# Kernel optimization log

Measured on AMD Instinct MI355X. Metric: run time of the kernel, lower is better.

## Reference

```python
import jax, jax.numpy as jnp
import numpy as np

N = 10000      # nodes
E = 160000     # edges (before self-loops)
F_IN = 128     # num_features
H1, D1 = 4, 256   # conv1: 4 heads x 256, concat -> 1024
D2 = 256          # conv2: 1 head x 256
NEG_SLOPE = 0.2


def setup_inputs() -> dict:
    key = jax.random.key(0)
    ks = jax.random.split(key, 12)
    def p(k, shape, fan):
        return jax.random.normal(k, shape, jnp.float32) / np.float32(np.sqrt(fan))
    return {
        "x": jax.random.normal(ks[0], (N, F_IN), jnp.float32),
        "edge_index": jax.random.randint(ks[1], (2, E), 0, N, jnp.int32),
        "W1": p(ks[2], (F_IN, H1 * D1), F_IN),
        "att_src1": p(ks[3], (H1, D1), D1),
        "att_dst1": p(ks[4], (H1, D1), D1),
        "b1": jnp.zeros((H1 * D1,), jnp.float32),
        "lin1_W": p(ks[5], (F_IN, H1 * D1), F_IN),
        "lin1_b": jnp.zeros((H1 * D1,), jnp.float32),
        "W2": p(ks[6], (H1 * D1, D2), H1 * D1),
        "att_src2": p(ks[7], (1, D2), D2),
        "att_dst2": p(ks[8], (1, D2), D2),
        "b2": jnp.zeros((D2,), jnp.float32),
        "lin2_W": p(ks[9], (H1 * D1, D2), H1 * D1),
        "lin2_b": jnp.zeros((D2,), jnp.float32),
    }


def gat_layer(x, src, dst, W, a_src, a_dst, b, heads, d):
    """PyG-style GATConv: transform, edgewise LeakyReLU attention,
    segment-softmax over destination neighborhoods, scatter-add, concat heads."""
    n = x.shape[0]
    h = (x @ W).reshape(n, heads, d)                       # [N, H, D]
    s_src = jnp.einsum('nhd,hd->nh', h, a_src)             # per-node scores
    s_dst = jnp.einsum('nhd,hd->nh', h, a_dst)
    e = jax.nn.leaky_relu(s_src[src] + s_dst[dst], NEG_SLOPE)   # [E, H]
    m = jax.ops.segment_max(e, dst, num_segments=n)        # stable softmax per dst
    p = jnp.exp(e - m[dst])
    z = jax.ops.segment_sum(p, dst, num_segments=n)
    alpha = p / (z[dst] + 1e-16)                           # [E, H]
    msg = h[src] * alpha[:, :, None]                       # [E, H, D]
    out = jax.ops.segment_sum(msg, dst, num_segments=n)    # [N, H, D]
    return out.reshape(n, heads * d) + b, alpha


def reference(x, edge_index, W1, att_src1, att_dst1, b1, lin1_W, lin1_b,
              W2, att_src2, att_dst2, b2, lin2_W, lin2_b):
    n = x.shape[0]
    loop = jnp.arange(n, dtype=edge_index.dtype)           # add self-loops (PyG default)
    src = jnp.concatenate([edge_index[0], loop])
    dst = jnp.concatenate([edge_index[1], loop])
    h1, alpha1 = gat_layer(x, src, dst, W1, att_src1, att_dst1, b1, H1, D1)
    h1 = jax.nn.elu(h1 + x @ lin1_W + lin1_b)              # conv1 + lin1 residual, ELU
    h2, _ = gat_layer(h1, src, dst, W2, att_src2, att_dst2, b2, 1, D2)
    out = h2 + h1 @ lin2_W + lin2_b                        # conv2 + lin2 residual
    return out, alpha1
```

## Files before the change

kernel.cpp:

```cpp
#include <hip/hip_runtime.h>
#include <hip/hip_bf16.h>
#include <math.h>

#define NN   10000
#define EE   160000
#define ETOT 170000
#define FIN  128
#define C1   1024
#define NH1  4
#define D1   256
#define D2   256

typedef __attribute__((ext_vector_type(8))) short bf16x8;
typedef __attribute__((ext_vector_type(4))) float f32x4;

__device__ __forceinline__ float b2f(unsigned short u)
{
    union { unsigned int i; float f; } c; c.i = (unsigned int)u << 16; return c.f;
}
__device__ __forceinline__ unsigned short f2b(float x)
{
    return __builtin_bit_cast(unsigned short, __float2bfloat16(x));
}
__device__ __forceinline__ void split1(float x, unsigned short &h, unsigned short &l)
{
    __hip_bfloat16 hb = __float2bfloat16(x);
    float r = x - __bfloat162float(hb);
    h = __builtin_bit_cast(unsigned short, hb);
    l = __builtin_bit_cast(unsigned short, __float2bfloat16(r));
}

__device__ __forceinline__ void split_A_body(const float* __restrict__ X,
                                             unsigned short* __restrict__ A2,
                                             int M, int K, int idx)
{
    int kq4 = K >> 2;
    if (idx >= M * kq4) return;
    int m = idx / kq4, kq = idx % kq4;
    float4 v = *(const float4*)&X[(size_t)m * K + kq * 4];
    ushort4 h, l;
    split1(v.x, h.x, l.x); split1(v.y, h.y, l.y);
    split1(v.z, h.z, l.z); split1(v.w, h.w, l.w);
    unsigned short* row = A2 + (size_t)m * (2 * K);
    *(ushort4*)&row[kq * 4]     = h;
    *(ushort4*)&row[K + kq * 4] = l;
}

__device__ __forceinline__ void split_Bt_body(const float* __restrict__ B0,
                                              const float* __restrict__ B1,
                                              int K, int N0, int Ntot,
                                              unsigned short* __restrict__ Bt, int idx)
{
    int total = Ntot * (K >> 2);
    if (idx >= total) return;
    int n = idx % Ntot;
    int kq = idx / Ntot;
    int k = kq * 4;
    const float* B; int nc, nb;
    if (n < N0) { B = B0; nc = n; nb = N0; }
    else        { B = B1; nc = n - N0; nb = Ntot - N0; }
    float v0 = B[(size_t)(k + 0) * nb + nc];
    float v1 = B[(size_t)(k + 1) * nb + nc];
    float v2 = B[(size_t)(k + 2) * nb + nc];
    float v3 = B[(size_t)(k + 3) * nb + nc];
    ushort4 h, l;
    split1(v0, h.x, l.x); split1(v1, h.y, l.y);
    split1(v2, h.z, l.z); split1(v3, h.w, l.w);
    unsigned short* row = Bt + (size_t)n * (3 * K);
    *(ushort4*)&row[k]         = h;
    *(ushort4*)&row[K + k]     = h;
    *(ushort4*)&row[2 * K + k] = l;
}

__device__ __forceinline__ void split_Bt1_body(const float* __restrict__ W1,
                                               const float* __restrict__ lin1W,
                                               unsigned short* __restrict__ Bt, int idx)
{
    if (idx >= 1024 * 64) return;
    int n = idx & 1023;
    int k = (idx >> 10) * 4;
    float v[4];
    #pragma unroll
    for (int i = 0; i < 4; ++i) {
        int kk = k + i;
        v[i] = (kk < 128) ? W1[(size_t)kk * C1 + n] : lin1W[(size_t)(kk - 128) * C1 + n];
    }
    ushort4 h, l;
    split1(v[0], h.x, l.x); split1(v[1], h.y, l.y);
    split1(v[2], h.z, l.z); split1(v[3], h.w, l.w);
    unsigned short* row = Bt + (size_t)n * 768;
    *(ushort4*)&row[k]       = h;
    *(ushort4*)&row[256 + k] = h;
    *(ushort4*)&row[512 + k] = l;
}

__global__ __launch_bounds__(256)
void prep(const float* __restrict__ x, unsigned short* __restrict__ A1stk,
          const float* __restrict__ W1, const float* __restrict__ lin1_W,
          unsigned short* __restrict__ Bt1,
          const float* __restrict__ W2, const float* __restrict__ lin2_W,
          unsigned short* __restrict__ Bt2,
          const int* __restrict__ dstp, int* __restrict__ cnt,
          const float* __restrict__ as1, const float* __restrict__ ad1,
          float* __restrict__ w1s, float* __restrict__ w1d,
          const float* __restrict__ as2, const float* __restrict__ ad2,
          float* __restrict__ v2s, float* __restrict__ v2d)
{
    const int b = blockIdx.x, t = threadIdx.x;
    const int w = t >> 6, lane = t & 63;
    if (b < 1250) {
        split_A_body(x, A1stk, NN, FIN, b * 256 + t);
    } else if (b < 1506) {
        split_Bt1_body(W1, lin1_W, Bt1, (b - 1250) * 256 + t);
    } else if (b < 2018) {
        split_Bt_body(W2, lin2_W, C1, D2, 512, Bt2, (b - 1506) * 256 + t);
    } else if (b < 2683) {
        int e = (b - 2018) * 256 + t;
        if (e < ETOT) {
            int d = (e < EE) ? dstp[e] : (e - EE);
            atomicAdd(&cnt[d], 1);
        }
    } else if (b < 2939) {
        int gw = (b - 2683) * 4 + w;
        int k = gw >> 3, rem = gw & 7, h = rem >> 1, issd = rem & 1;
        const float* a = issd ? ad1 : as1;
        float4 wv = *(const float4*)&W1[(size_t)k * C1 + h * 256 + lane * 4];
        float4 av = *(const float4*)&a[h * 256 + lane * 4];
        float s = wv.x * av.x + wv.y * av.y + wv.z * av.z + wv.w * av.w;
        #pragma unroll
        for (int off = 32; off; off >>= 1) s += __shfl_xor(s, off);
        if (lane == 0) (issd ? w1d : w1s)[k * 4 + h] = s;
    } else {
        int gw = (b - 2939) * 4 + w;
        int k = gw >> 1, issd = gw & 1;
        const float* a = issd ? ad2 : as2;
        float4 wv = *(const float4*)&W2[(size_t)k * D2 + lane * 4];
        float4 av = *(const float4*)&a[lane * 4];
        float s = wv.x * av.x + wv.y * av.y + wv.z * av.z + wv.w * av.w;
        #pragma unroll
        for (int off = 32; off; off >>= 1) s += __shfl_xor(s, off);
        if (lane == 0) (issd ? v2d : v2s)[k] = s;
    }
}

__device__ __forceinline__ void glds16(const void* g, void* l)
{
    __builtin_amdgcn_global_load_lds((const __attribute__((address_space(1))) void*)g,
                                     (__attribute__((address_space(3))) void*)l, 16, 0, 0);
}

__global__ __launch_bounds__(256)
void gemm_l1(const unsigned short* __restrict__ Apx,
             const unsigned short* __restrict__ Ax,
             const unsigned short* __restrict__ Bt,
             unsigned short* __restrict__ h1split,
             int M, const float* __restrict__ bias0, const float* __restrict__ bias1)
{
    constexpr int BM = 128, BN = 128, BK = 32;
    constexpr int FJ = 4, FI = 4;
    constexpr int SLOTS = 4, SMASK = 3, SWSH = 1;
    constexpr int RPC = 16, ACH = 8, CPW = 4;
    constexpr int ABUF = BM * BK, BBUF = BN * BK;
    __shared__ __align__(16) unsigned short sA[2 * ABUF];
    __shared__ __align__(16) unsigned short sB[2 * BBUF];
    const int tid = threadIdx.x, w = tid >> 6, lane = tid & 63;
    const int cpx = gridDim.x >> 3;
    const int t0 = (blockIdx.x & 7) * cpx + (blockIdx.x >> 3);
    const int m0 = (t0 >> 3) * BM;
    const int n0 = (t0 & 7) * BN;
    const int hsel = n0 >> 8;
    const int wm = w >> 1, wn = w & 1;
    f32x4 acc[FI][FJ] = {};

    const unsigned short *gx[CPW], *gpx[CPW], *gb[CPW];
    int lofs[CPW]; bool isa[CPW];
    {
        const int r = lane / SLOTS, sl = lane % SLOTS;
        const int ssl = sl ^ ((r >> SWSH) & SMASK);
        #pragma unroll
        for (int cc = 0; cc < CPW; ++cc) {
            int c = w * CPW + cc;
            if (c < ACH) {
                int gm = m0 + c * RPC + r; if (gm >= M) gm = M - 1;
                gx[cc]  = Ax  + (size_t)gm * 256 + ssl * 8;
                gpx[cc] = Apx + (size_t)gm * 1024 + hsel * 256 + ssl * 8;
                gb[cc]  = nullptr;
                lofs[cc] = c * 512;
                isa[cc] = true;
            } else {
                int gn = n0 + (c - ACH) * RPC + r;
                gx[cc] = gpx[cc] = nullptr;
                gb[cc] = Bt + (size_t)gn * 768 + ssl * 8;
                lofs[cc] = (c - ACH) * 512;
                isa[cc] = false;
            }
        }
    }

    const int rAl = wm * 64 + (lane & 15);
    const int rBl = wn * 64 + (lane & 15);
    const int sIdx = lane >> 4;
    const int nit = 768 / BK;
    int cur = 0;

    auto stage = [&](int kk, int buf) {
        int rr = kk >> 7;
        bool px = !(rr & 1);
        int off = px ? ((rr == 2) ? 128 : 0) : ((rr == 3) ? 128 : 0);
        int kin = kk & 127;
        #pragma unroll
        for (int cc = 0; cc < CPW; ++cc) {
            if (isa[cc]) glds16((px ? gpx[cc] : gx[cc]) + off + kin, sA + buf * ABUF + lofs[cc]);
            else         glds16(gb[cc] + kk,                         sB + buf * BBUF + lofs[cc]);
        }
    };

    stage(0, 0);
    __syncthreads();
    for (int it = 0; it < nit; ++it) {
        if (it + 1 < nit) stage((it + 1) * BK, cur ^ 1);
        const unsigned short* cA = sA + cur * ABUF;
        const unsigned short* cB = sB + cur * BBUF;
        bf16x8 av[FJ], bv[FI];
        #pragma unroll
        for (int f = 0; f < FI; ++f) {
            int row = rBl + f * 16;
            bv[f] = *(const bf16x8*)&cB[row * BK + ((sIdx ^ ((row >> SWSH) & SMASK)) << 3)];
        }
        #pragma unroll
        for (int f = 0; f < FJ; ++f) {
            int row = rAl + f * 16;
            av[f] = *(const bf16x8*)&cA[row * BK + ((sIdx ^ ((row >> SWSH) & SMASK)) << 3)];
        }
        #pragma unroll
        for (int fj = 0; fj < FJ; ++fj)
            #pragma unroll
            for (int fi = 0; fi < FI; ++fi)
                acc[fi][fj] = __builtin_amdgcn_mfma_f32_16x16x32_bf16(
                    bv[fi], av[fj], acc[fi][fj], 0, 0, 0);
        __syncthreads();
        cur ^= 1;
    }

    const int lrow = lane & 15;
    const int lcol = (lane >> 4) << 2;
    #pragma unroll
    for (int fj = 0; fj < FJ; ++fj) {
        int row = m0 + wm * 64 + fj * 16 + lrow;
        if (row >= M) continue;
        #pragma unroll
        for (int fi = 0; fi < FI; ++fi) {
            int col = n0 + wn * 64 + fi * 16 + lcol;
            f32x4 v = acc[fi][fj];
            const float4 g0 = *(const float4*)&bias0[col];
            const float4 g1 = *(const float4*)&bias1[col];
            v[0] += g0.x + g1.x; v[1] += g0.y + g1.y;
            v[2] += g0.z + g1.z; v[3] += g0.w + g1.w;
            #pragma unroll
            for (int i = 0; i < 4; ++i) v[i] = v[i] > 0.f ? v[i] : expm1f(v[i]);
            ushort4 hi, lo;
            split1(v[0], hi.x, lo.x); split1(v[1], hi.y, lo.y);
            split1(v[2], hi.z, lo.z); split1(v[3], hi.w, lo.w);
            unsigned short* orow = h1split + (size_t)row * 2048;
            *(ushort4*)&orow[col]        = hi;
            *(ushort4*)&orow[C1 + col]   = lo;
        }
    }
}

template<int BM, int BN, int WM, int WN, int BK>
__global__ __launch_bounds__(256)
void gemm_split(const unsigned short* __restrict__ A, int lda, int ka2,
                const unsigned short* __restrict__ Bt, int keff,
                unsigned short* __restrict__ outPb, float* __restrict__ outR,
                int M, int nsplit, int ldR, int ntn,
                const float* __restrict__ bias0, const float* __restrict__ bias1)
{
    constexpr int WTM  = BM / WM,  WTN = BN / WN;
    constexpr int FJ   = WTM / 16, FI  = WTN / 16;
    constexpr int KS   = BK / 32;
    constexpr int SLOTS = BK / 8;
    constexpr int SMASK = SLOTS - 1;
    constexpr int SWSH  = (BK == 32) ? 1 : 0;
    constexpr int RPC  = 512 / BK;
    constexpr int ACH  = BM / RPC;
    constexpr int NCH  = (BM + BN) / RPC;
    constexpr int CPW  = NCH / 4;
    constexpr int ABUF = BM * BK, BBUF = BN * BK;

    __shared__ __align__(16) unsigned short sA[2 * ABUF];
    __shared__ __align__(16) unsigned short sB[2 * BBUF];

    const int tid = threadIdx.x;
    const int w = tid >> 6, lane = tid & 63;

    const int cpx = gridDim.x >> 3;
    const int t0  = (blockIdx.x & 7) * cpx + (blockIdx.x >> 3);
    const int m0 = (t0 / ntn) * BM;
    const int n0 = (t0 % ntn) * BN;
    const int wm = w / WN, wn = w % WN;

    f32x4 acc[FI][FJ] = {};

    const unsigned short* gp[CPW];
    int lofs[CPW];
    bool isa[CPW];
    {
        const int r  = lane / SLOTS;
        const int sl = lane % SLOTS;
        const int ssl = sl ^ ((r >> SWSH) & SMASK);
        #pragma unroll
        for (int cc = 0; cc < CPW; ++cc) {
            int c = w * CPW + cc;
            if (c < ACH) {
                int gm = m0 + c * RPC + r; if (gm >= M) gm = M - 1;
                gp[cc]   = A + (size_t)gm * lda + ssl * 8;
                lofs[cc] = c * 512;
                isa[cc]  = true;
            } else {
                int gn = n0 + (c - ACH) * RPC + r;
                gp[cc]   = Bt + (size_t)gn * keff + ssl * 8;
                lofs[cc] = (c - ACH) * 512;
                isa[cc]  = false;
            }
        }
    }

    const int rAl = wm * WTM + (lane & 15);
    const int rBl = wn * WTN + (lane & 15);
    const int koff = (lane >> 4) * 8;
    const int nit = keff / BK;
    int cur = 0;

    #pragma unroll
    for (int cc = 0; cc < CPW; ++cc)
        glds16(gp[cc], (isa[cc] ? sA : sB) + lofs[cc]);
    __syncthreads();

    for (int it = 0; it < nit; ++it) {
        if (it + 1 < nit) {
            int kn = (it + 1) * BK;
            int kAn = (kn >= ka2) ? (kn - ka2) : kn;
            #pragma unroll
            for (int cc = 0; cc < CPW; ++cc) {
                unsigned short* dst = (isa[cc] ? sA + (cur ^ 1) * ABUF
                                               : sB + (cur ^ 1) * BBUF) + lofs[cc];
                glds16(gp[cc] + (isa[cc] ? kAn : kn), dst);
            }
        }
        const unsigned short* cA = sA + cur * ABUF;
        const unsigned short* cB = sB + cur * BBUF;
        #pragma unroll
        for (int ks = 0; ks < KS; ++ks) {
            const int sIdx = (ks * 32 + koff) >> 3;
            bf16x8 av[FJ], bv[FI];
            #pragma unroll
            for (int f = 0; f < FI; ++f) {
                int row = rBl + f * 16;
                bv[f] = *(const bf16x8*)&cB[row * BK + ((sIdx ^ ((row >> SWSH) & SMASK)) << 3)];
            }
            #pragma unroll
            for (int f = 0; f < FJ; ++f) {
                int row = rAl + f * 16;
                av[f] = *(const bf16x8*)&cA[row * BK + ((sIdx ^ ((row >> SWSH) & SMASK)) << 3)];
            }
            #pragma unroll
            for (int fj = 0; fj < FJ; ++fj)
                #pragma unroll
                for (int fi = 0; fi < FI; ++fi)
                    acc[fi][fj] = __builtin_amdgcn_mfma_f32_16x16x32_bf16(
                        bv[fi], av[fj], acc[fi][fj], 0, 0, 0);
        }
        __syncthreads();
        cur ^= 1;
    }

    const int lrow = lane & 15;
    const int lcol = (lane >> 4) << 2;
    #pragma unroll
    for (int fj = 0; fj < FJ; ++fj) {
        int row = m0 + wm * WTM + fj * 16 + lrow;
        if (row >= M) continue;
        #pragma unroll
        for (int fi = 0; fi < FI; ++fi) {
            int col = n0 + wn * WTN + fi * 16 + lcol;
            f32x4 v = acc[fi][fj];
            if (col < nsplit) {
                ushort4 o;
                o.x = f2b(v[0]); o.y = f2b(v[1]); o.z = f2b(v[2]); o.w = f2b(v[3]);
                *(ushort4*)&outPb[(size_t)row * nsplit + col] = o;
            } else {
                int c = col - nsplit;
                const float4 g0 = *(const float4*)&bias0[c];
                const float4 g1 = *(const float4*)&bias1[c];
                v[0] += g0.x + g1.x; v[1] += g0.y + g1.y;
                v[2] += g0.z + g1.z; v[3] += g0.w + g1.w;
                *(f32x4*)&outR[(size_t)row * ldR + c] = v;
            }
        }
    }
}

__global__ __launch_bounds__(256)
void s1_scores(const float* __restrict__ x, const float* __restrict__ w1s,
               const float* __restrict__ w1d, float* __restrict__ s_src,
               float* __restrict__ s_dst)
{
    const int n = blockIdx.x * 4 + (threadIdx.x >> 6);
    if (n >= NN) return;
    const int lane = threadIdx.x & 63;
    float2 xv = *(const float2*)&x[(size_t)n * FIN + lane * 2];
    float4 wa = *(const float4*)&w1s[(lane * 2) * 4];
    float4 wb = *(const float4*)&w1s[(lane * 2 + 1) * 4];
    float4 da = *(const float4*)&w1d[(lane * 2) * 4];
    float4 db = *(const float4*)&w1d[(lane * 2 + 1) * 4];
    float ss[4] = { xv.x * wa.x + xv.y * wb.x, xv.x * wa.y + xv.y * wb.y,
                    xv.x * wa.z + xv.y * wb.z, xv.x * wa.w + xv.y * wb.w };
    float sd[4] = { xv.x * da.x + xv.y * db.x, xv.x * da.y + xv.y * db.y,
                    xv.x * da.z + xv.y * db.z, xv.x * da.w + xv.y * db.w };
    #pragma unroll
    for (int off = 32; off; off >>= 1) {
        #pragma unroll
        for (int h = 0; h < 4; ++h) {
            ss[h] += __shfl_xor(ss[h], off);
            sd[h] += __shfl_xor(sd[h], off);
        }
    }
    if (lane == 0) {
        #pragma unroll
        for (int h = 0; h < 4; ++h) {
            s_src[n * NH1 + h] = ss[h];
            s_dst[n * NH1 + h] = sd[h];
        }
    }
}

__global__ __launch_bounds__(256)
void scores2(const unsigned short* __restrict__ h1split, const float* __restrict__ v2s,
             const float* __restrict__ v2d, float* __restrict__ s_src,
             float* __restrict__ s_dst)
{
    const int n = blockIdx.x * 4 + (threadIdx.x >> 6);
    if (n >= NN) return;
    const int lane = threadIdx.x & 63;
    const unsigned short* row = h1split + (size_t)n * 2048 + lane * 16;
    float ss = 0.f, sd = 0.f;
    #pragma unroll
    for (int q = 0; q < 16; ++q) {
        float hv = b2f(row[q]);
        ss += hv * v2s[lane * 16 + q];
        sd += hv * v2d[lane * 16 + q];
    }
    #pragma unroll
    for (int off = 32; off; off >>= 1) {
        ss += __shfl_xor(ss, off);
        sd += __shfl_xor(sd, off);
    }
    if (lane == 0) { s_src[n] = ss; s_dst[n] = sd; }
}

__global__ __launch_bounds__(1024)
void scan_kernel(const int* __restrict__ cnt, int* __restrict__ row_ptr)
{
    __shared__ int part[1024];
    const int t = threadIdx.x;
    int local[10];
    int s = 0;
    #pragma unroll
    for (int j = 0; j < 10; ++j) {
        int idx = t * 10 + j;
        local[j] = s;
        s += (idx < NN) ? cnt[idx] : 0;
    }
    part[t] = s;
    __syncthreads();
    for (int off = 1; off < 1024; off <<= 1) {
        int v = (t >= off) ? part[t - off] : 0;
        __syncthreads();
        part[t] += v;
        __syncthreads();
    }
    int prefix = (t > 0) ? part[t - 1] : 0;
    #pragma unroll
    for (int j = 0; j < 10; ++j) {
        int idx = t * 10 + j;
        if (idx < NN) row_ptr[idx] = prefix + local[j];
    }
    if (t == 0) row_ptr[NN] = ETOT;
}

__global__ void scatter_edges(const int* __restrict__ srcp, const int* __restrict__ dstp,
                              const int* __restrict__ row_ptr, int* __restrict__ fill,
                              int* __restrict__ csr_src, int* __restrict__ csr_eid,
                              int* __restrict__ csr_dst,
                              const float* __restrict__ s_src1,
                              const float* __restrict__ s_dst1,
                              float* __restrict__ sc1)
{
    int e = blockIdx.x * 256 + threadIdx.x;
    if (e >= ETOT) return;
    int s, d;
    if (e < EE) { s = srcp[e]; d = dstp[e]; } else { s = d = e - EE; }
    int pos = row_ptr[d] + atomicAdd(&fill[d], 1);
    csr_src[pos] = s;
    csr_eid[pos] = e;
    csr_dst[pos] = d;
    float4 ss = *(const float4*)&s_src1[s * 4];
    float4 dd = *(const float4*)&s_dst1[d * 4];
    float4 sc;
    sc.x = ss.x + dd.x; sc.y = ss.y + dd.y;
    sc.z = ss.z + dd.z; sc.w = ss.w + dd.w;
    sc.x = sc.x > 0.f ? sc.x : 0.2f * sc.x;
    sc.y = sc.y > 0.f ? sc.y : 0.2f * sc.y;
    sc.z = sc.z > 0.f ? sc.z : 0.2f * sc.z;
    sc.w = sc.w > 0.f ? sc.w : 0.2f * sc.w;
    *(float4*)&sc1[(size_t)pos * 4] = sc;
}

__global__ void sc2_kernel(const int* __restrict__ csr_src, const int* __restrict__ csr_dst,
                           const float* __restrict__ s_src2, const float* __restrict__ s_dst2,
                           float* __restrict__ sc2)
{
    int j = blockIdx.x * 256 + threadIdx.x;
    if (j >= ETOT) return;
    float sc = s_src2[csr_src[j]] + s_dst2[csr_dst[j]];
    sc2[j] = sc > 0.f ? sc : 0.2f * sc;
}

__global__ __launch_bounds__(256)
void mz1_alpha(const float* __restrict__ sc1, const int* __restrict__ row_ptr,
               const int* __restrict__ csr_eid, float* __restrict__ mz1,
               float* __restrict__ alpha_out)
{
    const int n = blockIdx.x * 4 + (threadIdx.x >> 6);
    if (n >= NN) return;
    const int lane = threadIdx.x & 63;
    const int start = row_ptr[n], end = row_ptr[n + 1];
    float4 m = make_float4(-1e30f, -1e30f, -1e30f, -1e30f);
    for (int i = start + lane; i < end; i += 64) {
        float4 s = *(const float4*)&sc1[(size_t)i * 4];
        m.x = fmaxf(m.x, s.x); m.y = fmaxf(m.y, s.y);
        m.z = fmaxf(m.z, s.z); m.w = fmaxf(m.w, s.w);
    }
    #pragma unroll
    for (int off = 32; off; off >>= 1) {
        m.x = fmaxf(m.x, __shfl_xor(m.x, off));
        m.y = fmaxf(m.y, __shfl_xor(m.y, off));
        m.z = fmaxf(m.z, __shfl_xor(m.z, off));
        m.w = fmaxf(m.w, __shfl_xor(m.w, off));
    }
    float4 z = make_float4(0.f, 0.f, 0.f, 0.f);
    for (int i = start + lane; i < end; i += 64) {
        float4 s = *(const float4*)&sc1[(size_t)i * 4];
        z.x += __expf(s.x - m.x); z.y += __expf(s.y - m.y);
        z.z += __expf(s.z - m.z); z.w += __expf(s.w - m.w);
    }
    #pragma unroll
    for (int off = 32; off; off >>= 1) {
        z.x += __shfl_xor(z.x, off); z.y += __shfl_xor(z.y, off);
        z.z += __shfl_xor(z.z, off); z.w += __shfl_xor(z.w, off);
    }
    float4 iz;
    iz.x = 1.f / (z.x + 1e-16f); iz.y = 1.f / (z.y + 1e-16f);
    iz.z = 1.f / (z.z + 1e-16f); iz.w = 1.f / (z.w + 1e-16f);
    if (lane == 0) {
        *(float4*)&mz1[(size_t)n * 8]     = m;
        *(float4*)&mz1[(size_t)n * 8 + 4] = iz;
    }
    for (int i = start + lane; i < end; i += 64) {
        float4 s = *(const float4*)&sc1[(size_t)i * 4];
        float4 a;
        a.x = __expf(s.x - m.x) * iz.x;
        a.y = __expf(s.y - m.y) * iz.y;
        a.z = __expf(s.z - m.z) * iz.z;
        a.w = __expf(s.w - m.w) * iz.w;
        *(float4*)&alpha_out[(size_t)csr_eid[i] * 4] = a;
    }
}

__global__ __launch_bounds__(256)
void mz2_kernel(const float* __restrict__ sc2, const int* __restrict__ row_ptr,
                float* __restrict__ mz2)
{
    const int n = blockIdx.x * 4 + (threadIdx.x >> 6);
    if (n >= NN) return;
    const int lane = threadIdx.x & 63;
    const int start = row_ptr[n], end = row_ptr[n + 1];
    float m = -1e30f;
    for (int i = start + lane; i < end; i += 64) m = fmaxf(m, sc2[i]);
    #pragma unroll
    for (int off = 32; off; off >>= 1) m = fmaxf(m, __shfl_xor(m, off));
    float z = 0.f;
    for (int i = start + lane; i < end; i += 64) z += __expf(sc2[i] - m);
    #pragma unroll
    for (int off = 32; off; off >>= 1) z += __shfl_xor(z, off);
    if (lane == 0) {
        mz2[(size_t)n * 2]     = m;
        mz2[(size_t)n * 2 + 1] = 1.f / (z + 1e-16f);
    }
}

__global__ __launch_bounds__(256)
void px_gather(const float* __restrict__ x, const float* __restrict__ sc1,
               const float* __restrict__ mz1, const int* __restrict__ row_ptr,
               const int* __restrict__ csr_src, unsigned short* __restrict__ Apx)
{
    __shared__ float red[4][16][33];
    const int n = blockIdx.x;
    const int t = threadIdx.x;
    const int w = t >> 6;
    const int lane = t & 63;
    const int start = row_ptr[n], end = row_ptr[n + 1];
    const float4 m  = *(const float4*)&mz1[(size_t)n * 8];
    const float4 iz = *(const float4*)&mz1[(size_t)n * 8 + 4];

    const int slot = w * 4 + (lane >> 4);
    const int g = lane & 15;
    float acc[4][8] = {};
    for (int i = start + slot; i < end; i += 16) {
        const int s = csr_src[i];
        float4 sv = *(const float4*)&sc1[(size_t)i * 4];
        const float a0 = __expf(sv.x - m.x) * iz.x;
        const float a1 = __expf(sv.y - m.y) * iz.y;
        const float a2 = __expf(sv.z - m.z) * iz.z;
        const float a3 = __expf(sv.w - m.w) * iz.w;
        const float* xr = &x[(size_t)s * FIN + g * 8];
        float4 v0 = *(const float4*)&xr[0];
        float4 v1 = *(const float4*)&xr[4];
        float vv[8] = { v0.x, v0.y, v0.z, v0.w, v1.x, v1.y, v1.z, v1.w };
        #pragma unroll
        for (int d = 0; d < 8; ++d) {
            acc[0][d] += a0 * vv[d];
            acc[1][d] += a1 * vv[d];
            acc[2][d] += a2 * vv[d];
            acc[3][d] += a3 * vv[d];
        }
    }
    #pragma unroll
    for (int off = 16; off <= 32; off <<= 1)
        #pragma unroll
        for (int h = 0; h < 4; ++h)
            #pragma unroll
            for (int d = 0; d < 8; ++d)
                acc[h][d] += __shfl_xor(acc[h][d], off);
    if ((lane >> 4) == 0) {
        #pragma unroll
        for (int h = 0; h < 4; ++h)
            #pragma unroll
            for (int d = 0; d < 8; ++d)
                red[w][g][h * 8 + d] = acc[h][d];
    }
    __syncthreads();
    if (lane < 16) {
        float sum[8];
        #pragma unroll
        for (int d = 0; d < 8; ++d)
            sum[d] = red[0][lane][w * 8 + d] + red[1][lane][w * 8 + d]
                   + red[2][lane][w * 8 + d] + red[3][lane][w * 8 + d];
        ushort4 hi0, hi1, lo0, lo1;
        split1(sum[0], hi0.x, lo0.x); split1(sum[1], hi0.y, lo0.y);
        split1(sum[2], hi0.z, lo0.z); split1(sum[3], hi0.w, lo0.w);
        split1(sum[4], hi1.x, lo1.x); split1(sum[5], hi1.y, lo1.y);
        split1(sum[6], hi1.z, lo1.z); split1(sum[7], hi1.w, lo1.w);
        unsigned short* orow = Apx + (size_t)n * 1024 + w * 256 + lane * 8;
        *(ushort4*)&orow[0]       = hi0;
        *(ushort4*)&orow[4]       = hi1;
        *(ushort4*)&orow[128]     = lo0;
        *(ushort4*)&orow[132]     = lo1;
    }
}

__global__ __launch_bounds__(64)
void aggregate2(const unsigned short* __restrict__ h2b, const float* __restrict__ sc2,
                const float* __restrict__ mz2, const int* __restrict__ row_ptr,
                const int* __restrict__ csr_src, const float* __restrict__ accin,
                float* __restrict__ out)
{
    const int n = blockIdx.x;
    const int t = threadIdx.x;
    const int start = row_ptr[n], end = row_ptr[n + 1];
    const float m    = mz2[(size_t)n * 2];
    const float invz = mz2[(size_t)n * 2 + 1];

    const int slot = t >> 4, g = t & 15;
    float acc[16] = {};
    for (int i = start + slot; i < end; i += 4) {
        const float a = __expf(sc2[i] - m) * invz;
        const unsigned short* vr = &h2b[(size_t)csr_src[i] * D2 + g * 16];
        bf16x8 u0 = *(const bf16x8*)&vr[0];
        bf16x8 u1 = *(const bf16x8*)&vr[8];
        #pragma unroll
        for (int d = 0; d < 8; ++d) {
            acc[d]     += a * b2f((unsigned short)u0[d]);
            acc[8 + d] += a * b2f((unsigned short)u1[d]);
        }
    }
    #pragma unroll
    for (int off = 16; off <= 32; off <<= 1)
        #pragma unroll
        for (int d = 0; d < 16; ++d)
            acc[d] += __shfl_xor(acc[d], off);
    if (slot == 0) {
        const float* br = &accin[(size_t)n * D2 + g * 16];
        float* orow = &out[(size_t)n * D2 + g * 16];
        #pragma unroll
        for (int q = 0; q < 4; ++q) {
            float4 b = *(const float4*)&br[q * 4];
            float4 r;
            r.x = acc[q * 4 + 0] + b.x; r.y = acc[q * 4 + 1] + b.y;
            r.z = acc[q * 4 + 2] + b.z; r.w = acc[q * 4 + 3] + b.w;
            *(float4*)&orow[q * 4] = r;
        }
    }
}

extern "C" void kernel_launch(void* const* d_in, const int* in_sizes, int n_in,
                              void* d_out, int out_size, void* d_ws, size_t ws_size,
                              hipStream_t stream)
{
    const float* x        = (const float*)d_in[0];
    const int*   ei       = (const int*)  d_in[1];
    const float* W1       = (const float*)d_in[2];
    const float* att_src1 = (const float*)d_in[3];
    const float* att_dst1 = (const float*)d_in[4];
    const float* b1       = (const float*)d_in[5];
    const float* lin1_W   = (const float*)d_in[6];
    const float* lin1_b   = (const float*)d_in[7];
    const float* W2       = (const float*)d_in[8];
    const float* att_src2 = (const float*)d_in[9];
    const float* att_dst2 = (const float*)d_in[10];
    const float* b2       = (const float*)d_in[11];
    const float* lin2_W   = (const float*)d_in[12];
    const float* lin2_b   = (const float*)d_in[13];
    const int* srcp = ei;
    const int* dstp = ei + EE;

    float* out    = (float*)d_out;
    float* alpha1 = out + (size_t)NN * D2;

    float* fw = (float*)d_ws;
    unsigned short* A1stk = (unsigned short*)fw; fw += (size_t)NN * 256 / 2;
    unsigned short* Apx   = (unsigned short*)fw; fw += (size_t)NN * 1024 / 2;
    unsigned short* A2stk = (unsigned short*)fw; fw += (size_t)NN * 2048 / 2;
    unsigned short* h2b   = (unsigned short*)fw; fw += (size_t)NN * 256 / 2;
    float* acc2   = fw;  fw += (size_t)NN * D2;
    unsigned short* Bt1 = (unsigned short*)fw; fw += (size_t)1024 * 768 / 2;
    unsigned short* Bt2 = (unsigned short*)fw; fw += (size_t)512 * 3072 / 2;
    float* w1s = fw; fw += 512;
    float* w1d = fw; fw += 512;
    float* v2s = fw; fw += 1024;
    float* v2d = fw; fw += 1024;
    float* s_src1 = fw; fw += NN * NH1;
    float* s_dst1 = fw; fw += NN * NH1;
    float* s_src2 = fw; fw += NN;
    float* s_dst2 = fw; fw += NN;
    float* sc1    = fw; fw += (size_t)ETOT * NH1;
    float* sc2    = fw; fw += ETOT;
    float* mz1    = fw; fw += (size_t)NN * 8;
    float* mz2    = fw; fw += (size_t)NN * 2;
    int* ip      = (int*)fw;
    int* cnt     = ip;  ip += NN;
    int* fill    = ip;  ip += NN;
    int* row_ptr = ip;  ip += NN + 4;
    int* csr_src = ip;  ip += ETOT;
    int* csr_eid = ip;  ip += ETOT;
    int* csr_dst = ip;  ip += ETOT;

    hipMemsetAsync(cnt, 0, 2 * NN * sizeof(int), stream);

    prep<<<3451, 256, 0, stream>>>(x, A1stk, W1, lin1_W, Bt1, W2, lin2_W, Bt2,
                                   dstp, cnt, att_src1, att_dst1, w1s, w1d,
                                   att_src2, att_dst2, v2s, v2d);

    s1_scores<<<(NN + 3) / 4, 256, 0, stream>>>(x, w1s, w1d, s_src1, s_dst1);

    scan_kernel<<<1, 1024, 0, stream>>>(cnt, row_ptr);
    scatter_edges<<<(ETOT + 255) / 256, 256, 0, stream>>>(srcp, dstp, row_ptr, fill,
                                                          csr_src, csr_eid, csr_dst,
                                                          s_src1, s_dst1, sc1);

    mz1_alpha<<<(NN + 3) / 4, 256, 0, stream>>>(sc1, row_ptr, csr_eid, mz1, alpha1);

    px_gather<<<NN, 256, 0, stream>>>(x, sc1, mz1, row_ptr, csr_src, Apx);

    gemm_l1<<<79 * 8, 256, 0, stream>>>(Apx, A1stk, Bt1, A2stk, NN, lin1_b, b1);

    scores2<<<(NN + 3) / 4, 256, 0, stream>>>(A2stk, v2s, v2d, s_src2, s_dst2);
    sc2_kernel<<<(ETOT + 255) / 256, 256, 0, stream>>>(csr_src, csr_dst, s_src2, s_dst2, sc2);
    mz2_kernel<<<(NN + 3) / 4, 256, 0, stream>>>(sc2, row_ptr, mz2);

    gemm_split<64, 64, 2, 2, 64><<<157 * 8, 256, 0, stream>>>(
        A2stk, 2 * C1, 2 * C1, Bt2, 3 * C1, h2b, acc2, NN, D2, D2, 8, lin2_b, b2);

    aggregate2<<<NN, 64, 0, stream>>>(h2b, sc2, mz2, row_ptr, csr_src, acc2, out);
}
```

Baseline: 248.8 us.

## Fuse layer-2 softmax into aggregation and merge scan into score kernel

Removes the separate sc2 and mz2 kernels and the csr_dst array by computing layer-2 edge scores, max and normaliser inside aggregate2, caching alphas in shared memory for the first 96 neighbours. The prefix scan is folded into the s1_scores launch as an extra block using 256 threads, and the second GEMM tile changes to 128x64. This cuts kernel launches and intermediate global traffic, but aggregate2 now re-reads csr_src and s_src several times per node, and the scan block runs alongside the score blocks in the same launch.

```diff
diff --git a/kernel.cpp b/kernel.cpp
--- a/kernel.cpp
+++ b/kernel.cpp
@@ -10,6 +10,7 @@
 #define NH1  4
 #define D1   256
 #define D2   256
+#define MAXD 96
 
 typedef __attribute__((ext_vector_type(8))) short bf16x8;
 typedef __attribute__((ext_vector_type(4))) float f32x4;
@@ -402,97 +403,72 @@
 }
 
 __global__ __launch_bounds__(256)
-void s1_scores(const float* __restrict__ x, const float* __restrict__ w1s,
-               const float* __restrict__ w1d, float* __restrict__ s_src,
-               float* __restrict__ s_dst)
-{
-    const int n = blockIdx.x * 4 + (threadIdx.x >> 6);
-    if (n >= NN) return;
-    const int lane = threadIdx.x & 63;
-    float2 xv = *(const float2*)&x[(size_t)n * FIN + lane * 2];
-    float4 wa = *(const float4*)&w1s[(lane * 2) * 4];
-    float4 wb = *(const float4*)&w1s[(lane * 2 + 1) * 4];
-    float4 da = *(const float4*)&w1d[(lane * 2) * 4];
-    float4 db = *(const float4*)&w1d[(lane * 2 + 1) * 4];
-    float ss[4] = { xv.x * wa.x + xv.y * wb.x, xv.x * wa.y + xv.y * wb.y,
-                    xv.x * wa.z + xv.y * wb.z, xv.x * wa.w + xv.y * wb.w };
-    float sd[4] = { xv.x * da.x + xv.y * db.x, xv.x * da.y + xv.y * db.y,
-                    xv.x * da.z + xv.y * db.z, xv.x * da.w + xv.y * db.w };
-    #pragma unroll
-    for (int off = 32; off; off >>= 1) {
-        #pragma unroll
-        for (int h = 0; h < 4; ++h) {
-            ss[h] += __shfl_xor(ss[h], off);
-            sd[h] += __shfl_xor(sd[h], off);
-        }
-    }
-    if (lane == 0) {
-        #pragma unroll
-        for (int h = 0; h < 4; ++h) {
-            s_src[n * NH1 + h] = ss[h];
-            s_dst[n * NH1 + h] = sd[h];
-        }
-    }
-}
-
-__global__ __launch_bounds__(256)
-void scores2(const unsigned short* __restrict__ h1split, const float* __restrict__ v2s,
-             const float* __restrict__ v2d, float* __restrict__ s_src,
-             float* __restrict__ s_dst)
-{
-    const int n = blockIdx.x * 4 + (threadIdx.x >> 6);
-    if (n >= NN) return;
-    const int lane = threadIdx.x & 63;
-    const unsigned short* row = h1split + (size_t)n * 2048 + lane * 16;
-    float ss = 0.f, sd = 0.f;
-    #pragma unroll
-    for (int q = 0; q < 16; ++q) {
-        float hv = b2f(row[q]);
-        ss += hv * v2s[lane * 16 + q];
-        sd += hv * v2d[lane * 16 + q];
-    }
-    #pragma unroll
-    for (int off = 32; off; off >>= 1) {
-        ss += __shfl_xor(ss, off);
-        sd += __shfl_xor(sd, off);
-    }
-    if (lane == 0) { s_src[n] = ss; s_dst[n] = sd; }
-}
-
-__global__ __launch_bounds__(1024)
-void scan_kernel(const int* __restrict__ cnt, int* __restrict__ row_ptr)
-{
-    __shared__ int part[1024];
-    const int t = threadIdx.x;
-    int local[10];
-    int s = 0;
-    #pragma unroll
-    for (int j = 0; j < 10; ++j) {
-        int idx = t * 10 + j;
-        local[j] = s;
-        s += (idx < NN) ? cnt[idx] : 0;
-    }
-    part[t] = s;
-    __syncthreads();
-    for (int off = 1; off < 1024; off <<= 1) {
-        int v = (t >= off) ? part[t - off] : 0;
+void s1_scores_scan(const float* __restrict__ x, const float* __restrict__ w1s,
+                    const float* __restrict__ w1d, float* __restrict__ s_src,
+                    float* __restrict__ s_dst,
+                    const int* __restrict__ cnt, int* __restrict__ row_ptr)
+{
+    const int b = blockIdx.x;
+    if (b < (NN + 3) / 4) {
+        const int n = b * 4 + (threadIdx.x >> 6);
+        if (n >= NN) return;
+        const int lane = threadIdx.x & 63;
+        float2 xv = *(const float2*)&x[(size_t)n * FIN + lane * 2];
+        float4 wa = *(const float4*)&w1s[(lane * 2) * 4];
+        float4 wb = *(const float4*)&w1s[(lane * 2 + 1) * 4];
+        float4 da = *(const float4*)&w1d[(lane * 2) * 4];
+        float4 db = *(const float4*)&w1d[(lane * 2 + 1) * 4];
+        float ss[4] = { xv.x * wa.x + xv.y * wb.x, xv.x * wa.y + xv.y * wb.y,
+                        xv.x * wa.z + xv.y * wb.z, xv.x * wa.w + xv.y * wb.w };
+        float sd[4] = { xv.x * da.x + xv.y * db.x, xv.x * da.y + xv.y * db.y,
+                        xv.x * da.z + xv.y * db.z, xv.x * da.w + xv.y * db.w };
+        #pragma unroll
+        for (int off = 32; off; off >>= 1) {
+            #pragma unroll
+            for (int h = 0; h < 4; ++h) {
+                ss[h] += __shfl_xor(ss[h], off);
+                sd[h] += __shfl_xor(sd[h], off);
+            }
+        }
+        if (lane == 0) {
+            #pragma unroll
+            for (int h = 0; h < 4; ++h) {
+                s_src[n * NH1 + h] = ss[h];
+                s_dst[n * NH1 + h] = sd[h];
+            }
+        }
+    } else {
+        __shared__ int part[256];
+        const int t = threadIdx.x;
+        int local[40];
+        int s = 0;
+        #pragma unroll
+        for (int j = 0; j < 40; ++j) {
+            int idx = t * 40 + j;
+            local[j] = s;
+            s += (idx < NN) ? cnt[idx] : 0;
+        }
+        part[t] = s;
         __syncthreads();
-        part[t] += v;
-        __syncthreads();
-    }
-    int prefix = (t > 0) ? part[t - 1] : 0;
-    #pragma unroll
-    for (int j = 0; j < 10; ++j) {
-        int idx = t * 10 + j;
-        if (idx < NN) row_ptr[idx] = prefix + local[j];
-    }
-    if (t == 0) row_ptr[NN] = ETOT;
+        for (int off = 1; off < 256; off <<= 1) {
+            int v = (t >= off) ? part[t - off] : 0;
+            __syncthreads();
+            part[t] += v;
+            __syncthreads();
+        }
+        int prefix = (t > 0) ? part[t - 1] : 0;
+        #pragma unroll
+        for (int j = 0; j < 40; ++j) {
+            int idx = t * 40 + j;
+            if (idx < NN) row_ptr[idx] = prefix + local[j];
+        }
+        if (t == 0) row_ptr[NN] = ETOT;
+    }
 }
 
 __global__ void scatter_edges(const int* __restrict__ srcp, const int* __restrict__ dstp,
                               const int* __restrict__ row_ptr, int* __restrict__ fill,
                               int* __restrict__ csr_src, int* __restrict__ csr_eid,
-                              int* __restrict__ csr_dst,
                               const float* __restrict__ s_src1,
                               const float* __restrict__ s_dst1,
                               float* __restrict__ sc1)
@@ -504,7 +480,6 @@
     int pos = row_ptr[d] + atomicAdd(&fill[d], 1);
     csr_src[pos] = s;
     csr_eid[pos] = e;
-    csr_dst[pos] = d;
     float4 ss = *(const float4*)&s_src1[s * 4];
     float4 dd = *(const float4*)&s_dst1[d * 4];
     float4 sc;
@@ -517,16 +492,6 @@
     *(float4*)&sc1[(size_t)pos * 4] = sc;
 }
 
-__global__ void sc2_kernel(const int* __restrict__ csr_src, const int* __restrict__ csr_dst,
-                           const float* __restrict__ s_src2, const float* __restrict__ s_dst2,
-                           float* __restrict__ sc2)
-{
-    int j = blockIdx.x * 256 + threadIdx.x;
-    if (j >= ETOT) return;
-    float sc = s_src2[csr_src[j]] + s_dst2[csr_dst[j]];
-    sc2[j] = sc > 0.f ? sc : 0.2f * sc;
-}
-
 __global__ __launch_bounds__(256)
 void mz1_alpha(const float* __restrict__ sc1, const int* __restrict__ row_ptr,
                const int* __restrict__ csr_eid, float* __restrict__ mz1,
@@ -575,28 +540,6 @@
         a.z = __expf(s.z - m.z) * iz.z;
         a.w = __expf(s.w - m.w) * iz.w;
         *(float4*)&alpha_out[(size_t)csr_eid[i] * 4] = a;
-    }
-}
-
-__global__ __launch_bounds__(256)
-void mz2_kernel(const float* __restrict__ sc2, const int* __restrict__ row_ptr,
-                float* __restrict__ mz2)
-{
-    const int n = blockIdx.x * 4 + (threadIdx.x >> 6);
-    if (n >= NN) return;
-    const int lane = threadIdx.x & 63;
-    const int start = row_ptr[n], end = row_ptr[n + 1];
-    float m = -1e30f;
-    for (int i = start + lane; i < end; i += 64) m = fmaxf(m, sc2[i]);
-    #pragma unroll
-    for (int off = 32; off; off >>= 1) m = fmaxf(m, __shfl_xor(m, off));
-    float z = 0.f;
-    for (int i = start + lane; i < end; i += 64) z += __expf(sc2[i] - m);
-    #pragma unroll
-    for (int off = 32; off; off >>= 1) z += __shfl_xor(z, off);
-    if (lane == 0) {
-        mz2[(size_t)n * 2]     = m;
-        mz2[(size_t)n * 2 + 1] = 1.f / (z + 1e-16f);
     }
 }
 
@@ -670,23 +613,81 @@
     }
 }
 
+__global__ __launch_bounds__(256)
+void scores2(const unsigned short* __restrict__ h1split, const float* __restrict__ v2s,
+             const float* __restrict__ v2d, float* __restrict__ s_src,
+             float* __restrict__ s_dst)
+{
+    const int n = blockIdx.x * 4 + (threadIdx.x >> 6);
+    if (n >= NN) return;
+    const int lane = threadIdx.x & 63;
+    const unsigned short* row = h1split + (size_t)n * 2048 + lane * 16;
+    float ss = 0.f, sd = 0.f;
+    #pragma unroll
+    for (int q = 0; q < 16; ++q) {
+        float hv = b2f(row[q]);
+        ss += hv * v2s[lane * 16 + q];
+        sd += hv * v2d[lane * 16 + q];
+    }
+    #pragma unroll
+    for (int off = 32; off; off >>= 1) {
+        ss += __shfl_xor(ss, off);
+        sd += __shfl_xor(sd, off);
+    }
+    if (lane == 0) { s_src[n] = ss; s_dst[n] = sd; }
+}
+
 __global__ __launch_bounds__(64)
-void aggregate2(const unsigned short* __restrict__ h2b, const float* __restrict__ sc2,
-                const float* __restrict__ mz2, const int* __restrict__ row_ptr,
-                const int* __restrict__ csr_src, const float* __restrict__ accin,
-                float* __restrict__ out)
-{
+void aggregate2(const unsigned short* __restrict__ h2b, const float* __restrict__ s_src,
+                const float* __restrict__ s_dst,
+                const int* __restrict__ row_ptr, const int* __restrict__ csr_src,
+                const float* __restrict__ accin, float* __restrict__ out)
+{
+    __shared__ float lalpha[MAXD];
     const int n = blockIdx.x;
     const int t = threadIdx.x;
     const int start = row_ptr[n], end = row_ptr[n + 1];
-    const float m    = mz2[(size_t)n * 2];
-    const float invz = mz2[(size_t)n * 2 + 1];
+    const float sd = s_dst[n];
+
+    float m = -1e30f;
+    for (int i = start + t; i < end; i += 64) {
+        float sc = s_src[csr_src[i]] + sd;
+        sc = sc > 0.f ? sc : 0.2f * sc;
+        m = fmaxf(m, sc);
+    }
+    #pragma unroll
+    for (int off = 32; off; off >>= 1) m = fmaxf(m, __shfl_xor(m, off));
+    float z = 0.f;
+    for (int i = start + t; i < end; i += 64) {
+        float sc = s_src[csr_src[i]] + sd;
+        sc = sc > 0.f ? sc : 0.2f * sc;
+        z += __expf(sc - m);
+    }
+    #pragma unroll
+    for (int off = 32; off; off >>= 1) z += __shfl_xor(z, off);
+    const float invz = 1.f / (z + 1e-16f);
+    for (int i = start + t; i < end; i += 64) {
+        float sc = s_src[csr_src[i]] + sd;
+        sc = sc > 0.f ? sc : 0.2f * sc;
+        int idx = i - start;
+        if (idx < MAXD) lalpha[idx] = __expf(sc - m) * invz;
+    }
+    __syncthreads();
 
     const int slot = t >> 4, g = t & 15;
     float acc[16] = {};
     for (int i = start + slot; i < end; i += 4) {
-        const float a = __expf(sc2[i] - m) * invz;
-        const unsigned short* vr = &h2b[(size_t)csr_src[i] * D2 + g * 16];
+        const int s = csr_src[i];
+        const int idx = i - start;
+        float a;
+        if (idx < MAXD) {
+            a = lalpha[idx];
+        } else {
+            float sc = s_src[s] + sd;
+            sc = sc > 0.f ? sc : 0.2f * sc;
+            a = __expf(sc - m) * invz;
+        }
+        const unsigned short* vr = &h2b[(size_t)s * D2 + g * 16];
         bf16x8 u0 = *(const bf16x8*)&vr[0];
         bf16x8 u1 = *(const bf16x8*)&vr[8];
         #pragma unroll
@@ -755,16 +756,13 @@
     float* s_src2 = fw; fw += NN;
     float* s_dst2 = fw; fw += NN;
     float* sc1    = fw; fw += (size_t)ETOT * NH1;
-    float* sc2    = fw; fw += ETOT;
     float* mz1    = fw; fw += (size_t)NN * 8;
-    float* mz2    = fw; fw += (size_t)NN * 2;
     int* ip      = (int*)fw;
     int* cnt     = ip;  ip += NN;
     int* fill    = ip;  ip += NN;
     int* row_ptr = ip;  ip += NN + 4;
     int* csr_src = ip;  ip += ETOT;
     int* csr_eid = ip;  ip += ETOT;
-    int* csr_dst = ip;  ip += ETOT;
 
     hipMemsetAsync(cnt, 0, 2 * NN * sizeof(int), stream);
 
@@ -772,11 +770,11 @@
                                    dstp, cnt, att_src1, att_dst1, w1s, w1d,
                                    att_src2, att_dst2, v2s, v2d);
 
-    s1_scores<<<(NN + 3) / 4, 256, 0, stream>>>(x, w1s, w1d, s_src1, s_dst1);
-
-    scan_kernel<<<1, 1024, 0, stream>>>(cnt, row_ptr);
+    s1_scores_scan<<<(NN + 3) / 4 + 1, 256, 0, stream>>>(x, w1s, w1d, s_src1, s_dst1,
+                                                         cnt, row_ptr);
+
     scatter_edges<<<(ETOT + 255) / 256, 256, 0, stream>>>(srcp, dstp, row_ptr, fill,
-                                                          csr_src, csr_eid, csr_dst,
+                                                          csr_src, csr_eid,
                                                           s_src1, s_dst1, sc1);
 
     mz1_alpha<<<(NN + 3) / 4, 256, 0, stream>>>(sc1, row_ptr, csr_eid, mz1, alpha1);
@@ -786,11 +784,9 @@
     gemm_l1<<<79 * 8, 256, 0, stream>>>(Apx, A1stk, Bt1, A2stk, NN, lin1_b, b1);
 
     scores2<<<(NN + 3) / 4, 256, 0, stream>>>(A2stk, v2s, v2d, s_src2, s_dst2);
-    sc2_kernel<<<(ETOT + 255) / 256, 256, 0, stream>>>(csr_src, csr_dst, s_src2, s_dst2, sc2);
-    mz2_kernel<<<(NN + 3) / 4, 256, 0, stream>>>(sc2, row_ptr, mz2);
-
-    gemm_split<64, 64, 2, 2, 64><<<157 * 8, 256, 0, stream>>>(
+
+    gemm_split<128, 64, 4, 1, 64><<<79 * 8, 256, 0, stream>>>(
         A2stk, 2 * C1, 2 * C1, Bt2, 3 * C1, h2b, acc2, NN, D2, D2, 8, lin2_b, b2);
 
-    aggregate2<<<NN, 64, 0, stream>>>(h2b, sc2, mz2, row_ptr, csr_src, acc2, out);
-}
+    aggregate2<<<NN, 64, 0, stream>>>(h2b, s_src2, s_dst2, row_ptr, csr_src, acc2, out);
+}
```

After: 218.9 us (median of 2 runs). 1.14x faster.
